# Kernel optimization log

Hardware: AMD Instinct MI355X
Metric: run time of the kernel (lower is better)

Reference implementation:

```python
import jax, jax.numpy as jnp
import numpy as np
from itertools import product

DIM = 384
HEADS = 8
DIM_HEAD = 64
INNER = HEADS * DIM_HEAD  # 512
KS = 3                    # kernel_size (attention window)
PAD = KS // 2
W_WIN = KS * KS           # 9
SCALE = DIM_HEAD ** -0.5


def setup_inputs() -> dict:
    key = jax.random.key(0)
    k1, k2, k3, k4, k5 = jax.random.split(key, 5)
    B, H, W = 4, 56, 56
    x = jax.random.normal(k1, (B, DIM, H, W), dtype=jnp.float32)
    # 1x1 conv weights stored as (out_ch, in_ch)
    Wq = jax.random.normal(k2, (INNER, DIM), dtype=jnp.float32) * (DIM ** -0.5)
    Wkv = jax.random.normal(k3, (2 * INNER, DIM), dtype=jnp.float32) * (DIM ** -0.5)
    Wo = jax.random.normal(k4, (DIM, INNER), dtype=jnp.float32) * (INNER ** -0.5)
    bo = jax.random.normal(k5, (DIM,), dtype=jnp.float32) * 0.01
    return {"x": x, "Wq": Wq, "Wkv": Wkv, "Wo": Wo, "bo": bo}


def _conv1x1(x, w):
    # x: (B,Cin,H,W), w: (Cout,Cin) -> (B,Cout,H,W)
    return jnp.einsum('bchw,oc->bohw', x, w)


def reference(x, Wq, Wkv, Wo, bo):
    B, C, H, W = x.shape
    q = _conv1x1(x, Wq)                       # (B, INNER, H, W)
    kv = _conv1x1(x, Wkv)                     # (B, 2*INNER, H, W)
    k, v = jnp.split(kv, 2, axis=1)
    # split channels heads-major, matching torch reshape (B, heads, dh, H, W)
    q = q.reshape(B, HEADS, DIM_HEAD, H, W)
    k = k.reshape(B, HEADS, DIM_HEAD, H, W)
    v = v.reshape(B, HEADS, DIM_HEAD, H, W)
    # zero-pad spatial dims (matches F.unfold zero padding: padded taps get logit 0)
    k_pad = jnp.pad(k, ((0, 0), (0, 0), (0, 0), (PAD, PAD), (PAD, PAD)))
    v_pad = jnp.pad(v, ((0, 0), (0, 0), (0, 0), (PAD, PAD), (PAD, PAD)))
    offsets = list(product(range(KS), range(KS)))  # row-major = unfold order
    # dots: (B, heads, H, W, w)
    dots = jnp.stack([
        jnp.einsum('bhdxy,bhdxy->bhxy', q, k_pad[:, :, :, i:i + H, j:j + W])
        for (i, j) in offsets
    ], axis=-1) * SCALE
    attn = jax.nn.softmax(dots, axis=-1)      # softmax over the 9-tap window
    # weighted sum of shifted v: (B, heads, dh, H, W)
    out = sum(
        attn[:, :, None, :, :, w_idx] * v_pad[:, :, :, i:i + H, j:j + W]
        for w_idx, (i, j) in enumerate(offsets)
    )
    out = out.reshape(B, INNER, H, W)
    return _conv1x1(out, Wo) + bo[None, :, None, None]
```

## Files before the change

kernel.cpp:

```cpp
#include <hip/hip_runtime.h>


#define HW 3136
#define WIMG 56
#define QKV_CH 1536
#define SCALE 0.125f
#define KSTR 72
#define NROWS 242
#define QKV_T 6422528

typedef __bf16 bf16x8_t __attribute__((ext_vector_type(8)));
typedef float f32x4_t __attribute__((ext_vector_type(4)));
typedef unsigned short ushort8 __attribute__((ext_vector_type(8)));

__device__ __forceinline__ float bf2f(unsigned short u) {
    return __uint_as_float(((unsigned int)u) << 16);
}
__device__ __forceinline__ unsigned short f2bf(float f) {
    unsigned int u = __float_as_uint(f);
    u += 0x7FFFu + ((u >> 16) & 1u);
    return (unsigned short)(u >> 16);
}

__device__ __forceinline__ void gll16(const unsigned short* g, unsigned short* l) {
    __builtin_amdgcn_global_load_lds(
        (const __attribute__((address_space(1))) unsigned int*)g,
        (__attribute__((address_space(3))) unsigned int*)l,
        16, 0, 0);
}

__global__ __launch_bounds__(256) void cvt_all(
    const float* __restrict__ x,
    const float* __restrict__ Wq, const float* __restrict__ Wkv,
    const float* __restrict__ Wo,
    unsigned short* __restrict__ xT,
    unsigned short* __restrict__ wT, unsigned short* __restrict__ wT3)
{
    __shared__ unsigned short Tl[64 * 36];
    const int bx = blockIdx.x;
    const int t = threadIdx.x;

    if (bx < 2400) {
        const int sblk = bx % 50;
        const int kblk = (bx / 50) % 12;
        const int b    = bx / 600;

        if (sblk == 49) {
            unsigned short* dst = xT + (((size_t)b * 25 + 24) * 12 + kblk) * 4096 + 2048;
            *reinterpret_cast<uint4*>(dst + t * 8) = (uint4){0, 0, 0, 0};
            return;
        }

        const float* xp = x + ((size_t)b * 384 + (size_t)kblk * 32) * HW + sblk * 64;
        const int c = t >> 3;
#pragma unroll
        for (int i = 0; i < 2; i++) {
            const int sc = (t & 7) + 8 * i;
            const float4 v = *reinterpret_cast<const float4*>(xp + (size_t)c * HW + sc * 4);
            const int s4 = sc * 4;
            Tl[(s4 + 0) * 36 + c] = f2bf(v.x);
            Tl[(s4 + 1) * 36 + c] = f2bf(v.y);
            Tl[(s4 + 2) * 36 + c] = f2bf(v.z);
            Tl[(s4 + 3) * 36 + c] = f2bf(v.w);
        }
        __syncthreads();

        const int row = t >> 2, gran = t & 3;
        const uint2 lo = *reinterpret_cast<const uint2*>(&Tl[row * 36 + gran * 8]);
        const uint2 hi = *reinterpret_cast<const uint2*>(&Tl[row * 36 + gran * 8 + 4]);
        uint4 o; o.x = lo.x; o.y = lo.y; o.z = hi.x; o.w = hi.y;
        unsigned short* dst = xT + (((size_t)b * 25 + (sblk >> 1)) * 12 + kblk) * 4096
                            + (sblk & 1) * 2048;
        *reinterpret_cast<uint4*>(dst + t * 8) = o;
        return;
    }

    const int i = (bx - 2400) * 256 + t;
    if (i < 73728) {
        const int g = i & 3;
        const int idx3 = i >> 2;
        const int o128 = idx3 & 127;
        const int rest = idx3 >> 7;
        const int kb = rest % 12, oblk = rest / 12;
        const int o = oblk * 128 + o128;
        const int k0 = kb * 32 + g * 8;
        const float* src = (o < 512) ? (Wq + (size_t)o * 384 + k0)
                                     : (Wkv + (size_t)(o - 512) * 384 + k0);
        const float4 v0 = *reinterpret_cast<const float4*>(src);
        const float4 v1 = *reinterpret_cast<const float4*>(src + 4);
        uint4 u;
        u.x = (unsigned int)f2bf(v0.x) | ((unsigned int)f2bf(v0.y) << 16);
        u.y = (unsigned int)f2bf(v0.z) | ((unsigned int)f2bf(v0.w) << 16);
        u.z = (unsigned int)f2bf(v1.x) | ((unsigned int)f2bf(v1.y) << 16);
        u.w = (unsigned int)f2bf(v1.z) | ((unsigned int)f2bf(v1.w) << 16);
        reinterpret_cast<uint4*>(wT)[i] = u;
    } else {
        const int j = i - 73728;
        const int g = j & 3;
        const int idx3 = j >> 2;
        const int o128 = idx3 & 127;
        const int rest = idx3 >> 7;
        const int kb = rest % 16, oblk = rest / 16;
        const int o = oblk * 128 + o128;
        const float* src = Wo + (size_t)o * 512 + kb * 32 + g * 8;
        const float4 v0 = *reinterpret_cast<const float4*>(src);
        const float4 v1 = *reinterpret_cast<const float4*>(src + 4);
        uint4 u;
        u.x = (unsigned int)f2bf(v0.x) | ((unsigned int)f2bf(v0.y) << 16);
        u.y = (unsigned int)f2bf(v0.z) | ((unsigned int)f2bf(v0.w) << 16);
        u.z = (unsigned int)f2bf(v1.x) | ((unsigned int)f2bf(v1.y) << 16);
        u.w = (unsigned int)f2bf(v1.z) | ((unsigned int)f2bf(v1.w) << 16);
        reinterpret_cast<uint4*>(wT3)[j] = u;
    }
}

__global__ __launch_bounds__(256) void gemm1(
    const unsigned short* __restrict__ xT,
    const unsigned short* __restrict__ wT,
    unsigned short* __restrict__ qkvT)
{
    __shared__ __align__(16) unsigned short A_lds[2][128 * 32];
    __shared__ __align__(16) unsigned short B_lds[2][128 * 32];

    const int lin = blockIdx.x;
    const int swz = (lin & 7) * 150 + (lin >> 3);
    const int sblk = swz % 25;
    const int oblk = (swz / 25) % 12;
    const int b    = swz / 300;

    const int t  = threadIdx.x;
    const int lane = t & 63, w = t >> 6;
    const int quad = lane >> 4, mrow = lane & 15;
    const int wm = w >> 1, wn = w & 1;

    const unsigned short* wsrc = wT + ((size_t)oblk * 12) * 4096;
    const unsigned short* xsrc = xT + (((size_t)b * 25 + sblk) * 12) * 4096;

    f32x4_t acc[4][4];
#pragma unroll
    for (int m = 0; m < 4; m++)
#pragma unroll
        for (int n = 0; n < 4; n++) acc[m][n] = (f32x4_t){0.f, 0.f, 0.f, 0.f};

    for (int kb = 0; kb < 6; kb++) {
        const size_t k0 = (size_t)(2 * kb) * 4096;
        const size_t k1 = (size_t)(2 * kb + 1) * 4096;
        __syncthreads();
        gll16(wsrc + k0 + t * 8,        A_lds[0] + t * 8);
        gll16(wsrc + k0 + 2048 + t * 8, A_lds[0] + 2048 + t * 8);
        gll16(wsrc + k1 + t * 8,        A_lds[1] + t * 8);
        gll16(wsrc + k1 + 2048 + t * 8, A_lds[1] + 2048 + t * 8);
        gll16(xsrc + k0 + t * 8,        B_lds[0] + t * 8);
        gll16(xsrc + k0 + 2048 + t * 8, B_lds[0] + 2048 + t * 8);
        gll16(xsrc + k1 + t * 8,        B_lds[1] + t * 8);
        gll16(xsrc + k1 + 2048 + t * 8, B_lds[1] + 2048 + t * 8);
        __syncthreads();

#pragma unroll
        for (int ks = 0; ks < 2; ks++) {
            bf16x8_t af[4], bfr[4];
#pragma unroll
            for (int m = 0; m < 4; m++)
                af[m] = *reinterpret_cast<const bf16x8_t*>(&A_lds[ks][(wm * 64 + m * 16 + mrow) * 32 + quad * 8]);
#pragma unroll
            for (int n = 0; n < 4; n++)
                bfr[n] = *reinterpret_cast<const bf16x8_t*>(&B_lds[ks][(wn * 64 + n * 16 + mrow) * 32 + quad * 8]);
#pragma unroll
            for (int m = 0; m < 4; m++)
#pragma unroll
                for (int n = 0; n < 4; n++)
                    acc[m][n] = __builtin_amdgcn_mfma_f32_16x16x32_bf16(af[m], bfr[n], acc[m][n], 0, 0, 0);
        }
    }

    const int which = oblk >> 2;
    const int hq = (oblk & 3) * 2 + wm;
    const int s0 = sblk * 128 + wn * 64;
    unsigned short* outb = qkvT + (size_t)which * QKV_T
                         + ((size_t)(b * 8 + hq) * HW) * 64;
#pragma unroll
    for (int m = 0; m < 4; m++) {
        const int d0 = m * 16 + quad * 4;
#pragma unroll
        for (int n = 0; n < 4; n++) {
            const int ss = s0 + n * 16 + mrow;
            if (ss < HW) {
                uint2 u;
                u.x = (unsigned int)f2bf(acc[m][n][0]) | ((unsigned int)f2bf(acc[m][n][1]) << 16);
                u.y = (unsigned int)f2bf(acc[m][n][2]) | ((unsigned int)f2bf(acc[m][n][3]) << 16);
                *reinterpret_cast<uint2*>(outb + (size_t)ss * 64 + d0) = u;
            }
        }
    }
}

__global__ __launch_bounds__(256) void natt2(
    const unsigned short* __restrict__ qkvT,
    unsigned short* __restrict__ aoT)
{
    __shared__ __align__(16) unsigned short KV[NROWS * KSTR];
    __shared__ float dred[9 * 2 * 128];

    const int lin = blockIdx.x;
    const int swz = (lin & 7) * 100 + (lin >> 3);
    const int sblk = swz % 25;
    const int h = (swz / 25) & 7;
    const int b = swz / 200;

    const int t = threadIdx.x;
    const int p  = t & 127;
    const int dq = t >> 7;
    const int s0 = sblk * 128;
    const int s  = s0 + p;
    const int sc = min(s, HW - 1);
    const int y  = sc / WIMG, xx = sc % WIMG;

    const unsigned short* qg = qkvT + ((size_t)(b * 8 + h) * HW) * 64;
    const unsigned short* kg = qg + (size_t)QKV_T;
    const unsigned short* vg = qg + (size_t)(2 * QKV_T);

#pragma unroll
    for (int i = 0; i < 8; i++) {
        const int f = i * 256 + t;
        if (f < NROWS * 8) {
            const int row = f >> 3, c8 = f & 7;
            int srow = s0 - 57 + row;
            srow = min(max(srow, 0), HW - 1);
            const uint4 k4 = *reinterpret_cast<const uint4*>(kg + (size_t)srow * 64 + c8 * 8);
            *reinterpret_cast<uint4*>(&KV[row * KSTR + c8 * 8]) = k4;
        }
    }

    int   roff[9];
    float msk[9];
#pragma unroll
    for (int ty = 0; ty < 3; ty++)
#pragma unroll
        for (int tx = 0; tx < 3; tx++) {
            const int tap = ty * 3 + tx;
            const int ny = y + ty - 1, nx = xx + tx - 1;
            const bool v = (ny >= 0) && (ny < WIMG) && (nx >= 0) && (nx < WIMG);
            roff[tap] = (v ? ((ty - 1) * WIMG + (tx - 1)) : 0) * KSTR;
            msk[tap]  = v ? 1.f : 0.f;
        }

    float qv[32];
#pragma unroll
    for (int c = 0; c < 4; c++) {
        const uint4 q4 = *reinterpret_cast<const uint4*>(qg + (size_t)sc * 64 + dq * 32 + c * 8);
        qv[c*8+0] = bf2f((unsigned short)(q4.x & 0xffff)); qv[c*8+1] = bf2f((unsigned short)(q4.x >> 16));
        qv[c*8+2] = bf2f((unsigned short)(q4.y & 0xffff)); qv[c*8+3] = bf2f((unsigned short)(q4.y >> 16));
        qv[c*8+4] = bf2f((unsigned short)(q4.z & 0xffff)); qv[c*8+5] = bf2f((unsigned short)(q4.z >> 16));
        qv[c*8+6] = bf2f((unsigned short)(q4.w & 0xffff)); qv[c*8+7] = bf2f((unsigned short)(q4.w >> 16));
    }

    __syncthreads();

    const int rbase = (57 + p) * KSTR + dq * 32;

    float dots[9];
#pragma unroll
    for (int tp = 0; tp < 9; tp++) dots[tp] = 0.f;
#pragma unroll
    for (int ch = 0; ch < 4; ch++) {
#pragma unroll
        for (int tp = 0; tp < 9; tp++) {
            const ushort8 kk = *reinterpret_cast<const ushort8*>(&KV[rbase + roff[tp] + ch * 8]);
#pragma unroll
            for (int j = 0; j < 8; j++)
                dots[tp] += qv[ch * 8 + j] * bf2f(kk[j]);
        }
    }

    __syncthreads();

#pragma unroll
    for (int tp = 0; tp < 9; tp++) dred[(tp * 2 + dq) * 128 + p] = dots[tp];
#pragma unroll
    for (int i = 0; i < 8; i++) {
        const int f = i * 256 + t;
        if (f < NROWS * 8) {
            const int row = f >> 3, c8 = f & 7;
            int srow = s0 - 57 + row;
            srow = min(max(srow, 0), HW - 1);
            const uint4 v4 = *reinterpret_cast<const uint4*>(vg + (size_t)srow * 64 + c8 * 8);
            *reinterpret_cast<uint4*>(&KV[row * KSTR + c8 * 8]) = v4;
        }
    }

    __syncthreads();

    float mx = -1e30f, dt[9];
#pragma unroll
    for (int tp = 0; tp < 9; tp++) {
        const float sum = dred[(tp * 2 + 0) * 128 + p] + dred[(tp * 2 + 1) * 128 + p];
        dt[tp] = msk[tp] * (sum * SCALE);
        mx = fmaxf(mx, dt[tp]);
    }
    float se = 0.f, w9[9];
#pragma unroll
    for (int tp = 0; tp < 9; tp++) { w9[tp] = __expf(dt[tp] - mx); se += w9[tp]; }
    const float inv = 1.f / se;
#pragma unroll
    for (int tp = 0; tp < 9; tp++) w9[tp] *= inv * msk[tp];

    float o[32];
#pragma unroll
    for (int dd = 0; dd < 32; dd++) o[dd] = 0.f;
#pragma unroll
    for (int ch = 0; ch < 4; ch++) {
        ushort8 vfr[9];
#pragma unroll
        for (int tp = 0; tp < 9; tp++)
            vfr[tp] = *reinterpret_cast<const ushort8*>(&KV[rbase + roff[tp] + ch * 8]);
#pragma unroll
        for (int j = 0; j < 8; j++)
#pragma unroll
            for (int tp = 0; tp < 9; tp++)
                o[ch * 8 + j] += w9[tp] * bf2f(vfr[tp][j]);
    }

    if (s < HW) {
        __align__(16) unsigned short ov[32];
#pragma unroll
        for (int dd = 0; dd < 32; dd++) ov[dd] = f2bf(o[dd]);
        unsigned short* dst = aoT + (((size_t)(b * 49 + (s >> 6))) * 16 + (h * 2 + dq)) * 2048
                            + (s & 63) * 32;
        *reinterpret_cast<uint4*>(dst)      = *reinterpret_cast<const uint4*>(ov);
        *reinterpret_cast<uint4*>(dst + 8)  = *reinterpret_cast<const uint4*>(ov + 8);
        *reinterpret_cast<uint4*>(dst + 16) = *reinterpret_cast<const uint4*>(ov + 16);
        *reinterpret_cast<uint4*>(dst + 24) = *reinterpret_cast<const uint4*>(ov + 24);
    }
}

__global__ __launch_bounds__(256) void gemm3(
    const unsigned short* __restrict__ aoT,
    const unsigned short* __restrict__ wT3,
    const float* __restrict__ bias,
    float* __restrict__ out)
{
    __shared__ __align__(16) unsigned short A_lds[2][128 * 32];
    __shared__ __align__(16) unsigned short B_lds[2][64 * 32];

    const int lin = blockIdx.x;
    const int xcd = lin & 7, idx = lin >> 3;
    const int wid = (xcd < 4) ? (xcd * 74 + idx) : (296 + (xcd - 4) * 73 + idx);
    const int oblk = wid % 3;
    const int sblk = (wid / 3) % 49;
    const int b    = wid / 147;

    const int t  = threadIdx.x;
    const int lane = t & 63, w = t >> 6;
    const int quad = lane >> 4, mrow = lane & 15;
    const int wm = w >> 1, wn = w & 1;

    const unsigned short* asrc = wT3 + (size_t)oblk * 16 * 4096;
    const unsigned short* bsrc = aoT + ((size_t)(b * 49 + sblk)) * 16 * 2048;

    f32x4_t acc[4][2];
#pragma unroll
    for (int m = 0; m < 4; m++)
#pragma unroll
        for (int n = 0; n < 2; n++) acc[m][n] = (f32x4_t){0.f, 0.f, 0.f, 0.f};

    for (int kb = 0; kb < 8; kb++) {
        const size_t a0 = (size_t)(2 * kb) * 4096;
        const size_t a1 = (size_t)(2 * kb + 1) * 4096;
        const size_t b0 = (size_t)(2 * kb) * 2048;
        const size_t b1 = (size_t)(2 * kb + 1) * 2048;
        __syncthreads();
        gll16(asrc + a0 + t * 8,        A_lds[0] + t * 8);
        gll16(asrc + a0 + 2048 + t * 8, A_lds[0] + 2048 + t * 8);
        gll16(asrc + a1 + t * 8,        A_lds[1] + t * 8);
        gll16(asrc + a1 + 2048 + t * 8, A_lds[1] + 2048 + t * 8);
        gll16(bsrc + b0 + t * 8,        B_lds[0] + t * 8);
        gll16(bsrc + b1 + t * 8,        B_lds[1] + t * 8);
        __syncthreads();

#pragma unroll
        for (int ks = 0; ks < 2; ks++) {
            bf16x8_t af[4], bfr[2];
#pragma unroll
            for (int m = 0; m < 4; m++)
                af[m] = *reinterpret_cast<const bf16x8_t*>(&A_lds[ks][(wm * 64 + m * 16 + mrow) * 32 + quad * 8]);
#pragma unroll
            for (int n = 0; n < 2; n++)
                bfr[n] = *reinterpret_cast<const bf16x8_t*>(&B_lds[ks][(wn * 32 + n * 16 + mrow) * 32 + quad * 8]);
#pragma unroll
            for (int m = 0; m < 4; m++)
#pragma unroll
                for (int n = 0; n < 2; n++)
                    acc[m][n] = __builtin_amdgcn_mfma_f32_16x16x32_bf16(af[m], bfr[n], acc[m][n], 0, 0, 0);
        }
    }

    const int o0 = oblk * 128 + wm * 64;
    const int s0 = sblk * 64 + wn * 32;
    float* outb = out + (size_t)b * 384 * HW;
#pragma unroll
    for (int m = 0; m < 4; m++)
#pragma unroll
        for (int n = 0; n < 2; n++) {
            const int ss = s0 + n * 16 + mrow;
#pragma unroll
            for (int r = 0; r < 4; r++) {
                const int oo = o0 + m * 16 + quad * 4 + r;
                outb[(size_t)oo * HW + ss] = acc[m][n][r] + bias[oo];
            }
        }
}

extern "C" void kernel_launch(void* const* d_in, const int* in_sizes, int n_in,
                              void* d_out, int out_size, void* d_ws, size_t ws_size,
                              hipStream_t stream) {
    const float* x   = (const float*)d_in[0];
    const float* Wq  = (const float*)d_in[1];
    const float* Wkv = (const float*)d_in[2];
    const float* Wo  = (const float*)d_in[3];
    const float* bo  = (const float*)d_in[4];
    float* out = (float*)d_out;

    unsigned short* xT   = (unsigned short*)d_ws;
    unsigned short* wT   = xT + (size_t)4915200;
    unsigned short* wT3  = wT + (size_t)589824;
    unsigned short* qkvT = wT3 + (size_t)196608;
    unsigned short* aoT  = qkvT + (size_t)(3 * QKV_T);

    cvt_all<<<dim3(2784), 256, 0, stream>>>(x, Wq, Wkv, Wo, xT, wT, wT3);

    gemm1<<<dim3(1200), 256, 0, stream>>>(xT, wT, qkvT);
    natt2<<<dim3(800), 256, 0, stream>>>(qkvT, aoT);
    gemm3<<<dim3(588), 256, 0, stream>>>(aoT, wT3, bo, out);
}
```

Before: 133.2 us.

## Double-buffer LDS tiles in both GEMM kernels to overlap loads with MFMA

Result: no change. 134.3 us (+0.8%).

```diff
diff --git a/kernel.cpp b/kernel.cpp
--- a/kernel.cpp
+++ b/kernel.cpp
@@ -142,35 +142,39 @@
 #pragma unroll
         for (int n = 0; n < 4; n++) acc[m][n] = (f32x4_t){0.f, 0.f, 0.f, 0.f};
 
-    for (int kb = 0; kb < 6; kb++) {
-        const size_t k0 = (size_t)(2 * kb) * 4096;
-        const size_t k1 = (size_t)(2 * kb + 1) * 4096;
-        __syncthreads();
-        gll16(wsrc + k0 + t * 8,        A_lds[0] + t * 8);
-        gll16(wsrc + k0 + 2048 + t * 8, A_lds[0] + 2048 + t * 8);
-        gll16(wsrc + k1 + t * 8,        A_lds[1] + t * 8);
-        gll16(wsrc + k1 + 2048 + t * 8, A_lds[1] + 2048 + t * 8);
-        gll16(xsrc + k0 + t * 8,        B_lds[0] + t * 8);
-        gll16(xsrc + k0 + 2048 + t * 8, B_lds[0] + 2048 + t * 8);
-        gll16(xsrc + k1 + t * 8,        B_lds[1] + t * 8);
-        gll16(xsrc + k1 + 2048 + t * 8, B_lds[1] + 2048 + t * 8);
-        __syncthreads();
-
-#pragma unroll
-        for (int ks = 0; ks < 2; ks++) {
-            bf16x8_t af[4], bfr[4];
-#pragma unroll
-            for (int m = 0; m < 4; m++)
-                af[m] = *reinterpret_cast<const bf16x8_t*>(&A_lds[ks][(wm * 64 + m * 16 + mrow) * 32 + quad * 8]);
+    gll16(wsrc + t * 8,        A_lds[0] + t * 8);
+    gll16(wsrc + 2048 + t * 8, A_lds[0] + 2048 + t * 8);
+    gll16(xsrc + t * 8,        B_lds[0] + t * 8);
+    gll16(xsrc + 2048 + t * 8, B_lds[0] + 2048 + t * 8);
+    __syncthreads();
+
+    for (int kb = 0; kb < 12; kb++) {
+        const int p = kb & 1;
+        bf16x8_t af[4], bfr[4];
+#pragma unroll
+        for (int m = 0; m < 4; m++)
+            af[m] = *reinterpret_cast<const bf16x8_t*>(&A_lds[p][(wm * 64 + m * 16 + mrow) * 32 + quad * 8]);
+#pragma unroll
+        for (int n = 0; n < 4; n++)
+            bfr[n] = *reinterpret_cast<const bf16x8_t*>(&B_lds[p][(wn * 64 + n * 16 + mrow) * 32 + quad * 8]);
+
+        if (kb + 1 < 12) {
+            const size_t ko = (size_t)(kb + 1) * 4096;
+            gll16(wsrc + ko + t * 8,        A_lds[p ^ 1] + t * 8);
+            gll16(wsrc + ko + 2048 + t * 8, A_lds[p ^ 1] + 2048 + t * 8);
+            gll16(xsrc + ko + t * 8,        B_lds[p ^ 1] + t * 8);
+            gll16(xsrc + ko + 2048 + t * 8, B_lds[p ^ 1] + 2048 + t * 8);
+        }
+
+#pragma unroll
+        for (int m = 0; m < 4; m++)
 #pragma unroll
             for (int n = 0; n < 4; n++)
-                bfr[n] = *reinterpret_cast<const bf16x8_t*>(&B_lds[ks][(wn * 64 + n * 16 + mrow) * 32 + quad * 8]);
-#pragma unroll
-            for (int m = 0; m < 4; m++)
-#pragma unroll
-                for (int n = 0; n < 4; n++)
-                    acc[m][n] = __builtin_amdgcn_mfma_f32_16x16x32_bf16(af[m], bfr[n], acc[m][n], 0, 0, 0);
-        }
+                acc[m][n] = __builtin_amdgcn_mfma_f32_16x16x32_bf16(af[m], bfr[n], acc[m][n], 0, 0, 0);
+
+        asm volatile("s_waitcnt vmcnt(0)" ::: "memory");
+        __builtin_amdgcn_s_barrier();
+        __builtin_amdgcn_sched_barrier(0);
     }
 
     const int which = oblk >> 2;
@@ -363,35 +367,38 @@
 #pragma unroll
         for (int n = 0; n < 2; n++) acc[m][n] = (f32x4_t){0.f, 0.f, 0.f, 0.f};
 
-    for (int kb = 0; kb < 8; kb++) {
-        const size_t a0 = (size_t)(2 * kb) * 4096;
-        const size_t a1 = (size_t)(2 * kb + 1) * 4096;
-        const size_t b0 = (size_t)(2 * kb) * 2048;
-        const size_t b1 = (size_t)(2 * kb + 1) * 2048;
-        __syncthreads();
-        gll16(asrc + a0 + t * 8,        A_lds[0] + t * 8);
-        gll16(asrc + a0 + 2048 + t * 8, A_lds[0] + 2048 + t * 8);
-        gll16(asrc + a1 + t * 8,        A_lds[1] + t * 8);
-        gll16(asrc + a1 + 2048 + t * 8, A_lds[1] + 2048 + t * 8);
-        gll16(bsrc + b0 + t * 8,        B_lds[0] + t * 8);
-        gll16(bsrc + b1 + t * 8,        B_lds[1] + t * 8);
-        __syncthreads();
-
-#pragma unroll
-        for (int ks = 0; ks < 2; ks++) {
-            bf16x8_t af[4], bfr[2];
-#pragma unroll
-            for (int m = 0; m < 4; m++)
-                af[m] = *reinterpret_cast<const bf16x8_t*>(&A_lds[ks][(wm * 64 + m * 16 + mrow) * 32 + quad * 8]);
+    gll16(asrc + t * 8,        A_lds[0] + t * 8);
+    gll16(asrc + 2048 + t * 8, A_lds[0] + 2048 + t * 8);
+    gll16(bsrc + t * 8,        B_lds[0] + t * 8);
+    __syncthreads();
+
+    for (int kb = 0; kb < 16; kb++) {
+        const int p = kb & 1;
+        bf16x8_t af[4], bfr[2];
+#pragma unroll
+        for (int m = 0; m < 4; m++)
+            af[m] = *reinterpret_cast<const bf16x8_t*>(&A_lds[p][(wm * 64 + m * 16 + mrow) * 32 + quad * 8]);
+#pragma unroll
+        for (int n = 0; n < 2; n++)
+            bfr[n] = *reinterpret_cast<const bf16x8_t*>(&B_lds[p][(wn * 32 + n * 16 + mrow) * 32 + quad * 8]);
+
+        if (kb + 1 < 16) {
+            const size_t ao = (size_t)(kb + 1) * 4096;
+            const size_t bo = (size_t)(kb + 1) * 2048;
+            gll16(asrc + ao + t * 8,        A_lds[p ^ 1] + t * 8);
+            gll16(asrc + ao + 2048 + t * 8, A_lds[p ^ 1] + 2048 + t * 8);
+            gll16(bsrc + bo + t * 8,        B_lds[p ^ 1] + t * 8);
+        }
+
+#pragma unroll
+        for (int m = 0; m < 4; m++)
 #pragma unroll
             for (int n = 0; n < 2; n++)
-                bfr[n] = *reinterpret_cast<const bf16x8_t*>(&B_lds[ks][(wn * 32 + n * 16 + mrow) * 32 + quad * 8]);
-#pragma unroll
-            for (int m = 0; m < 4; m++)
-#pragma unroll
-                for (int n = 0; n < 2; n++)
-                    acc[m][n] = __builtin_amdgcn_mfma_f32_16x16x32_bf16(af[m], bfr[n], acc[m][n], 0, 0, 0);
-        }
+                acc[m][n] = __builtin_amdgcn_mfma_f32_16x16x32_bf16(af[m], bfr[n], acc[m][n], 0, 0, 0);
+
+        asm volatile("s_waitcnt vmcnt(0)" ::: "memory");
+        __builtin_amdgcn_s_barrier();
+        __builtin_amdgcn_sched_barrier(0);
     }
 
     const int o0 = oblk * 128 + wm * 64;
```
